# Optimization experiments

Measured on AMD Instinct MI355X. Metric: run time of the kernel, lower is better.

Reference implementation:

```python
import jax, jax.numpy as jnp
import numpy as np
from functools import partial

NUM_GROUP = 512   # S
GROUP_SIZE = 32   # K
BN_EPS = 1e-5
STD_EPS = 1e-5


def fps(xyz, n_samples):
    # xyz: [N,3] -> indices [n_samples] (farthest point sampling, start at idx 0)
    N = xyz.shape[0]
    def body(carry, _):
        dists, last = carry
        d = jnp.sum((xyz - xyz[last]) ** 2, axis=-1)
        dists = jnp.minimum(dists, d)
        nxt = jnp.argmax(dists).astype(jnp.int32)
        return (dists, nxt), last
    init = (jnp.full((N,), jnp.inf, xyz.dtype), jnp.array(0, jnp.int32))
    _, idx = jax.lax.scan(body, init, None, length=n_samples)
    return idx


def knn_idx(xyz, center, k):
    # xyz [N,3], center [S,3] -> k nearest neighbor indices [S,k]
    d2 = (jnp.sum(center ** 2, -1)[:, None] + jnp.sum(xyz ** 2, -1)[None, :]
          - 2.0 * center @ xyz.T)
    _, idx = jax.lax.top_k(-d2, k)
    return idx


def conv1(x, W, b):
    # 1x1 Conv1d: x [M,Cin,L], W [Cout,Cin] -> [M,Cout,L]
    return jnp.einsum('oc,mcl->mol', W, x) + b[None, :, None]


def bn(x, g, b):
    # BatchNorm1d eval mode with running_mean=0, running_var=1
    scale = g / jnp.sqrt(1.0 + BN_EPS)
    return x * scale[None, :, None] + b[None, :, None]


def res_block(x, W1, b1, g1, bb1, W2, b2, g2, bb2):
    # ConvBNReLURes1D, res_expansion=1.0
    h = jax.nn.relu(bn(conv1(x, W1, b1), g1, bb1))
    h = bn(conv1(h, W2, b2), g2, bb2)
    return jax.nn.relu(h + x)


def reference(xyz, alpha, beta, Wt, bt, gt, bbt,
              Wpre1, bpre1, gpre1, bbpre1, Wpre2, bpre2, gpre2, bbpre2,
              Wpos1, bpos1, gpos1, bbpos1, Wpos2, bpos2, gpos2, bbpos2):
    B, N, _ = xyz.shape
    S, K = NUM_GROUP, GROUP_SIZE
    C = Wt.shape[0]

    # ---- LocalGrouper: FPS + KNN + gather + normalize ----
    c_idx = jax.vmap(partial(fps, n_samples=S))(xyz)          # [B,S]
    center = jax.vmap(lambda p, i: p[i])(xyz, c_idx)          # [B,S,3]
    n_idx = jax.vmap(partial(knn_idx, k=K))(xyz, center)      # [B,S,K]
    nbr = jax.vmap(lambda p, i: p[i])(xyz, n_idx)             # [B,S,K,3]

    mean = center[:, :, None, :]
    diff = nbr - mean
    std = jnp.std(diff.reshape(B, -1), axis=-1, ddof=1).reshape(B, 1, 1, 1)
    nbr = alpha * (diff / (std + STD_EPS)) + beta
    grouped = jnp.concatenate(
        [nbr, jnp.broadcast_to(mean, (B, S, K, 3))], axis=-1)  # [B,S,K,6]

    # ---- Extraction ----
    x = grouped.transpose(0, 1, 3, 2).reshape(B * S, 6, K)     # [B*S,6,K]
    h = jax.nn.relu(bn(conv1(x, Wt, bt), gt, bbt))             # [B*S,C,K]
    h = res_block(h, Wpre1, bpre1, gpre1, bbpre1, Wpre2, bpre2, gpre2, bbpre2)
    pooled = jnp.max(h, axis=-1)                               # [B*S,C]
    feat = pooled.reshape(B, S, C).transpose(0, 2, 1)          # [B,C,S]
    feat = res_block(feat, Wpos1, bpos1, gpos1, bbpos1, Wpos2, bpos2, gpos2, bbpos2)
    return feat.transpose(0, 2, 1)                             # [B,S,C]


def setup_inputs() -> dict:
    key = jax.random.key(0)
    ks = jax.random.split(key, 12)
    B, N, C = 8, 8192, 384
    s6 = 1.0 / np.sqrt(6.0)
    sc = 1.0 / np.sqrt(C)
    return {
        'xyz': jax.random.normal(ks[0], (B, N, 3), jnp.float32),
        'alpha': jnp.ones((1, 1, 1, 3), jnp.float32),
        'beta': jnp.zeros((1, 1, 1, 3), jnp.float32),
        'Wt': jax.random.normal(ks[1], (C, 6), jnp.float32) * s6,
        'bt': jax.random.normal(ks[2], (C,), jnp.float32) * 0.02,
        'gt': jnp.ones((C,), jnp.float32), 'bbt': jnp.zeros((C,), jnp.float32),
        'Wpre1': jax.random.normal(ks[3], (C, C), jnp.float32) * sc,
        'bpre1': jax.random.normal(ks[4], (C,), jnp.float32) * 0.02,
        'gpre1': jnp.ones((C,), jnp.float32), 'bbpre1': jnp.zeros((C,), jnp.float32),
        'Wpre2': jax.random.normal(ks[5], (C, C), jnp.float32) * sc,
        'bpre2': jax.random.normal(ks[6], (C,), jnp.float32) * 0.02,
        'gpre2': jnp.ones((C,), jnp.float32), 'bbpre2': jnp.zeros((C,), jnp.float32),
        'Wpos1': jax.random.normal(ks[7], (C, C), jnp.float32) * sc,
        'bpos1': jax.random.normal(ks[8], (C,), jnp.float32) * 0.02,
        'gpos1': jnp.ones((C,), jnp.float32), 'bbpos1': jnp.zeros((C,), jnp.float32),
        'Wpos2': jax.random.normal(ks[9], (C, C), jnp.float32) * sc,
        'bpos2': jax.random.normal(ks[10], (C,), jnp.float32) * 0.02,
        'gpos2': jnp.ones((C,), jnp.float32), 'bbpos2': jnp.zeros((C,), jnp.float32),
    }
```

## Files before the change

kernel.cpp:

```cpp
#include <hip/hip_runtime.h>
#include <hip/hip_bf16.h>
#include <math.h>

typedef __bf16 bf16x8 __attribute__((ext_vector_type(8)));
typedef float f32x4 __attribute__((ext_vector_type(4)));
typedef float f32x2 __attribute__((ext_vector_type(2)));

#define NPTS 8192
#define SGRP 512
#define KNBR 32
#define CCH 384
#define LDSP 392

static __device__ __forceinline__ unsigned short f2b(float f) {
  union { float f; unsigned u; } v; v.f = f;
  return (unsigned short)((v.u + 0x7fffu + ((v.u >> 16) & 1u)) >> 16);
}
static __device__ __forceinline__ float b2f(unsigned short u) {
  union { unsigned u; float f; } v; v.u = ((unsigned)u) << 16;
  return v.f;
}
static __device__ __forceinline__ unsigned pk2(float a, float b) {
  return (unsigned)f2b(a) | ((unsigned)f2b(b) << 16);
}

#define DPPMAX(v, ctrl) \
  fmaxf((v), __int_as_float(__builtin_amdgcn_update_dpp(0, __float_as_int(v), (ctrl), 0xf, 0xf, false)))
#define DPPMIN(v, ctrl) \
  fminf((v), __int_as_float(__builtin_amdgcn_update_dpp(0x7f800000, __float_as_int(v), (ctrl), 0xf, 0xf, false)))

struct FoldArgs {
  const float *W, *b, *g, *bb;
  unsigned short* Wd;
  float* bd;
};
__global__ void fold4_bf16(FoldArgs a0, FoldArgs a1, FoldArgs a2, FoldArgs a3) {
  FoldArgs a = (blockIdx.y == 0) ? a0 : (blockIdx.y == 1) ? a1 : (blockIdx.y == 2) ? a2 : a3;
  int o = blockIdx.x;
  float sc = a.g[o] / sqrtf(1.0f + 1e-5f);
  for (int c = threadIdx.x; c < CCH; c += blockDim.x)
    a.Wd[o * CCH + c] = f2b(a.W[o * CCH + c] * sc);
  if (threadIdx.x == 0) a.bd[o] = a.b[o] * sc + a.bb[o];
}
__global__ void fold_w_f32(const float* __restrict__ W, const float* __restrict__ b,
                           const float* __restrict__ g, const float* __restrict__ bb,
                           float* __restrict__ Wd, float* __restrict__ bd, int Cin) {
  int o = blockIdx.x;
  float sc = g[o] / sqrtf(1.0f + 1e-5f);
  for (int c = threadIdx.x; c < Cin; c += blockDim.x)
    Wd[o * Cin + c] = W[o * Cin + c] * sc;
  if (threadIdx.x == 0) bd[o] = b[o] * sc + bb[o];
}

__global__ __launch_bounds__(1024)
void fps_kernel(const float* __restrict__ xyz, int* __restrict__ cIdx) {
  #pragma clang fp contract(off)
  __shared__ float xs[NPTS], ys[NPTS], zs[NPTS];
  __shared__ float slotV[2][16];
  __shared__ unsigned slotI[2][16];
  const int tid = threadIdx.x, lane = tid & 63, wid = tid >> 6;
  const int b = blockIdx.x;
  const float* xb = xyz + (size_t)b * NPTS * 3;

  f32x2 X2[4], Y2[4], Z2[4], D2[4];
  {
    const float4* s = (const float4*)xb + tid * 6;
    float4 t0 = s[0], t1 = s[1], t2 = s[2], t3 = s[3], t4 = s[4], t5 = s[5];
    X2[0] = (f32x2){t0.x, t0.w}; Y2[0] = (f32x2){t0.y, t1.x}; Z2[0] = (f32x2){t0.z, t1.y};
    X2[1] = (f32x2){t1.z, t2.y}; Y2[1] = (f32x2){t1.w, t2.z}; Z2[1] = (f32x2){t2.x, t2.w};
    X2[2] = (f32x2){t3.x, t3.w}; Y2[2] = (f32x2){t3.y, t4.x}; Z2[2] = (f32x2){t3.z, t4.y};
    X2[3] = (f32x2){t4.z, t5.y}; Y2[3] = (f32x2){t4.w, t5.z}; Z2[3] = (f32x2){t5.x, t5.w};
  }
  #pragma unroll
  for (int j = 0; j < 4; ++j) {
    int p = tid * 8 + j * 2;
    xs[p] = X2[j].x; ys[p] = Y2[j].x; zs[p] = Z2[j].x;
    xs[p + 1] = X2[j].y; ys[p + 1] = Y2[j].y; zs[p + 1] = Z2[j].y;
    D2[j] = (f32x2){__builtin_inff(), __builtin_inff()};
  }
  if (tid == 0) cIdx[b * SGRP] = 0;
  __syncthreads();
  float cx = xs[0], cy = ys[0], cz = zs[0];
  const int tbase = tid * 8;

  for (int step = 1; step < SGRP; ++step) {
    const int par = step & 1;
    const f32x2 cxv = (f32x2){cx, cx}, cyv = (f32x2){cy, cy}, czv = (f32x2){cz, cz};
    float bv = -1.0f; int bi = 0;
    #pragma unroll
    for (int j = 0; j < 4; ++j) {
      f32x2 dx = X2[j] - cxv, dy = Y2[j] - cyv, dz = Z2[j] - czv;
      f32x2 d = (dx * dx + dy * dy) + dz * dz;
      f32x2 nd = __builtin_elementwise_min(D2[j], d);
      D2[j] = nd;
      if (nd.x > bv) { bv = nd.x; bi = tbase + 2 * j; }
      if (nd.y > bv) { bv = nd.y; bi = tbase + 2 * j + 1; }
    }
    float m = bv;
    m = DPPMAX(m, 0x111); m = DPPMAX(m, 0x112); m = DPPMAX(m, 0x114);
    m = DPPMAX(m, 0x118); m = DPPMAX(m, 0x142); m = DPPMAX(m, 0x143);
    float wmax = __uint_as_float(__builtin_amdgcn_readlane(__float_as_uint(m), 63));
    unsigned long long msk = __ballot(bv == wmax);
    int srcLane = (int)__builtin_ctzll(msk);
    unsigned wbi = (unsigned)__builtin_amdgcn_readlane(bi, srcLane);
    if (lane == 0) { slotV[par][wid] = wmax; slotI[par][wid] = wbi; }
    __syncthreads();
    float sv = slotV[par][lane & 15];
    unsigned si = slotI[par][lane & 15];
    float g = sv;
    g = DPPMAX(g, 0x111); g = DPPMAX(g, 0x112); g = DPPMAX(g, 0x114);
    g = DPPMAX(g, 0x118);
    float gm = __uint_as_float(__builtin_amdgcn_readlane(__float_as_uint(g), 15));
    int l0 = (int)__builtin_ctzll(__ballot(sv == gm));
    unsigned gi = (unsigned)__builtin_amdgcn_readlane((int)si, l0);
    if (tid == 0) cIdx[b * SGRP + step] = (int)gi;
    cx = xs[gi]; cy = ys[gi]; cz = zs[gi];
  }
}

__global__ __launch_bounds__(512) void knn_kernel(const float* __restrict__ xyz,
                                                  const int* __restrict__ cIdx,
                                                  float* __restrict__ nbrDiff,
                                                  float* __restrict__ ctrW,
                                                  float* __restrict__ partials) {
  #pragma clang fp contract(off)
  __shared__ unsigned long long keyBuf[4];
  __shared__ int winners[KNBR];
  const int cid = blockIdx.x;
  const int b = cid >> 9;
  const int tid = threadIdx.x;
  const int lane = tid & 63;
  const float* xb = xyz + (size_t)b * NPTS * 3;
  const int cI = cIdx[cid];
  const float cx = xb[cI * 3], cy = xb[cI * 3 + 1], cz = xb[cI * 3 + 2];
  const float cs = (cx * cx + cy * cy) + cz * cz;

  float d2[16];
  float mv = __builtin_inff(); int mi = 0;
  #pragma unroll
  for (int j = 0; j < 16; ++j) {
    int p = tid + (j << 9);
    float x = xb[p * 3], y = xb[p * 3 + 1], z = xb[p * 3 + 2];
    float ps = (x * x + y * y) + z * z;
    float dot = (cx * x + cy * y) + cz * z;
    d2[j] = (cs + ps) - 2.0f * dot;
    if (d2[j] < mv) { mv = d2[j]; mi = p; }
  }
  if (tid < 4) keyBuf[tid] = 0xFFFFFFFFFFFFFFFFull;
  __syncthreads();

  for (int it = 0; it < KNBR; ++it) {
    if (tid == 0) keyBuf[(it + 2) & 3] = 0xFFFFFFFFFFFFFFFFull;
    float m = mv;
    m = DPPMIN(m, 0x111); m = DPPMIN(m, 0x112); m = DPPMIN(m, 0x114);
    m = DPPMIN(m, 0x118); m = DPPMIN(m, 0x142); m = DPPMIN(m, 0x143);
    float wmin = __uint_as_float(__builtin_amdgcn_readlane(__float_as_uint(m), 63));
    unsigned long long msk = __ballot(mv == wmin);
    int src = (int)__builtin_ctzll(msk);
    int wbi = __builtin_amdgcn_readlane(mi, src);
    if (__builtin_popcountll(msk) > 1) {
      unsigned long long rest = msk & (msk - 1);
      while (rest) {
        int l = (int)__builtin_ctzll(rest);
        int cand = __builtin_amdgcn_readlane(mi, l);
        if (cand < wbi) wbi = cand;
        rest &= rest - 1;
      }
    }
    if (lane == 0) {
      unsigned u = __float_as_uint(wmin);
      unsigned mm = u ^ (unsigned)(((int)u >> 31) | 0x80000000);
      unsigned long long key = (((unsigned long long)mm) << 32) | (unsigned long long)(unsigned)wbi;
      atomicMin(&keyBuf[it & 3], key);
    }
    __syncthreads();
    unsigned long long k = keyBuf[it & 3];
    int wi = (int)(k & 0x1FFFu);
    if (tid == 0) winners[it] = wi;
    if (tid == (wi & 511)) {
      #pragma unroll
      for (int j = 0; j < 16; ++j)
        if (wi == tid + (j << 9)) d2[j] = __builtin_inff();
      mv = __builtin_inff(); mi = 0;
      #pragma unroll
      for (int j = 0; j < 16; ++j)
        if (d2[j] < mv) { mv = d2[j]; mi = tid + (j << 9); }
    }
  }
  __syncthreads();

  float sum = 0.f, sq = 0.f;
  if (tid < KNBR) {
    int w = winners[tid];
    float dx = xb[w * 3] - cx, dy = xb[w * 3 + 1] - cy, dz = xb[w * 3 + 2] - cz;
    size_t o = ((size_t)cid * KNBR + tid) * 3;
    nbrDiff[o + 0] = dx; nbrDiff[o + 1] = dy; nbrDiff[o + 2] = dz;
    sum = (dx + dy) + dz;
    sq = (dx * dx + dy * dy) + dz * dz;
  }
  if (tid < 64) {
    #pragma unroll
    for (int s = 1; s < 64; s <<= 1) { sum += __shfl_xor(sum, s); sq += __shfl_xor(sq, s); }
    if (tid == 0) { partials[cid * 2] = sum; partials[cid * 2 + 1] = sq; }
  }
  if (tid < 3) ctrW[(size_t)cid * 3 + tid] = xb[cI * 3 + tid];
}

__global__ __launch_bounds__(256) void std_kernel(const float* __restrict__ partials,
                                                  float* __restrict__ stdv) {
  __shared__ double sd[256], sq[256];
  const int b = blockIdx.x, t = threadIdx.x;
  int i0 = (b * 512 + t) * 2;
  sd[t] = (double)partials[i0] + (double)partials[i0 + 512];
  sq[t] = (double)partials[i0 + 1] + (double)partials[i0 + 513];
  for (int st = 128; st > 0; st >>= 1) {
    __syncthreads();
    if (t < st) { sd[t] += sd[t + st]; sq[t] += sq[t + st]; }
  }
  if (t == 0) {
    double n = (double)(SGRP * KNBR * 3);
    double mean = sd[0] / n;
    double var = (sq[0] - sd[0] * mean) / (n - 1.0);
    stdv[b] = (float)sqrt(var);
  }
}

static __device__ __forceinline__ void gemm_half(const unsigned short* __restrict__ W,
                                                 const unsigned short* ht,
                                                 int oBase, int n0, int r16, int g4,
                                                 f32x4 acc[3][4]) {
  for (int ks = 0; ks < 12; ++ks) {
    const int kOff = ks * 32 + g4 * 8;
    bf16x8 a[3], bb[4];
    #pragma unroll
    for (int i = 0; i < 3; ++i)
      a[i] = *(const bf16x8*)(W + (size_t)(oBase + i * 16 + r16) * CCH + kOff);
    #pragma unroll
    for (int j = 0; j < 4; ++j)
      bb[j] = *(const bf16x8*)(ht + (n0 + j * 16 + r16) * LDSP + kOff);
    #pragma unroll
    for (int i = 0; i < 3; ++i) {
      #pragma unroll
      for (int j = 0; j < 4; ++j)
        acc[i][j] = __builtin_amdgcn_mfma_f32_16x16x32_bf16(a[i], bb[j], acc[i][j], 0, 0, 0);
    }
  }
}

__global__ __launch_bounds__(512) void group_mlp_kernel(
    const float* __restrict__ alpha, const float* __restrict__ beta,
    const float* __restrict__ WtF, const float* __restrict__ btF,
    const unsigned short* __restrict__ W1, const float* __restrict__ b1,
    const unsigned short* __restrict__ W2, const float* __restrict__ b2,
    const float* __restrict__ nbrDiff, const float* __restrict__ ctrW,
    const float* __restrict__ stdv, unsigned short* __restrict__ feat) {
  __shared__ unsigned short ht[128 * LDSP];
  __shared__ float xtw[128 * 8];
  __shared__ float wtl[CCH * 6];
  __shared__ float btl[CCH];

  const int tid = threadIdx.x;
  const int lane = tid & 63, wid = tid >> 6;
  const int r16 = lane & 15, g4 = lane >> 4;
  const int bid = blockIdx.x;
  const int b = bid >> 7;
  const int sBase = (bid & 127) << 2;

  for (int i = tid; i < CCH * 6; i += 512) wtl[i] = WtF[i];
  for (int i = tid; i < CCH; i += 512) btl[i] = btF[i];

  const float inv = 1.0f / (stdv[b] + 1e-5f);
  if (tid < 128) {
    int g = tid >> 5, kk = tid & 31;
    int cid = b * SGRP + sBase + g;
    const float* nb = nbrDiff + ((size_t)cid * KNBR + kk) * 3;
    const float* cc = ctrW + (size_t)cid * 3;
    #pragma unroll
    for (int c = 0; c < 3; ++c) {
      xtw[tid * 8 + c] = alpha[c] * (nb[c] * inv) + beta[c];
      xtw[tid * 8 + 3 + c] = cc[c];
    }
  }
  __syncthreads();

  {
    int l = tid & 127, oi = tid >> 7;
    float xv[6];
    #pragma unroll
    for (int c = 0; c < 6; ++c) xv[c] = xtw[l * 8 + c];
    for (int j = 0; j < 96; ++j) {
      int o = oi * 96 + j;
      float v = btl[o];
      #pragma unroll
      for (int c = 0; c < 6; ++c) v += wtl[o * 6 + c] * xv[c];
      ht[l * LDSP + o] = f2b(fmaxf(v, 0.0f));
    }
  }
  __syncthreads();

  const int oBase = wid * 48;

  for (int half = 0; half < 2; ++half) {
    const int n0 = half * 64;
    f32x4 acc[3][4];
    #pragma unroll
    for (int i = 0; i < 3; ++i) {
      #pragma unroll
      for (int j = 0; j < 4; ++j) acc[i][j] = (f32x4){0.f, 0.f, 0.f, 0.f};
    }
    gemm_half(W1, ht, oBase, n0, r16, g4, acc);
    __syncthreads();
    #pragma unroll
    for (int i = 0; i < 3; ++i) {
      int o4 = oBase + i * 16 + g4 * 4;
      float bs0 = b1[o4], bs1 = b1[o4 + 1], bs2 = b1[o4 + 2], bs3 = b1[o4 + 3];
      #pragma unroll
      for (int j = 0; j < 4; ++j) {
        int row = n0 + j * 16 + r16;
        unsigned u0 = pk2(fmaxf(acc[i][j][0] + bs0, 0.f), fmaxf(acc[i][j][1] + bs1, 0.f));
        unsigned u1 = pk2(fmaxf(acc[i][j][2] + bs2, 0.f), fmaxf(acc[i][j][3] + bs3, 0.f));
        *(uint2*)(ht + row * LDSP + o4) = make_uint2(u0, u1);
      }
    }
    __syncthreads();
  }

  for (int half = 0; half < 2; ++half) {
    const int n0 = half * 64;
    f32x4 acc[3][4];
    #pragma unroll
    for (int i = 0; i < 3; ++i) {
      #pragma unroll
      for (int j = 0; j < 4; ++j) acc[i][j] = (f32x4){0.f, 0.f, 0.f, 0.f};
    }
    gemm_half(W2, ht, oBase, n0, r16, g4, acc);

    float bias2[3][4];
    #pragma unroll
    for (int i = 0; i < 3; ++i) {
      int o4 = oBase + i * 16 + g4 * 4;
      #pragma unroll
      for (int r = 0; r < 4; ++r) bias2[i][r] = b2[o4 + r];
    }
    float mx[3][2][4];
    #pragma unroll
    for (int i = 0; i < 3; ++i) {
      #pragma unroll
      for (int gg = 0; gg < 2; ++gg) {
        #pragma unroll
        for (int r = 0; r < 4; ++r) mx[i][gg][r] = 0.f;
      }
    }
    #pragma unroll
    for (int j = 0; j < 4; ++j) {
      int l = n0 + j * 16 + r16;
      float xv[6];
      #pragma unroll
      for (int c = 0; c < 6; ++c) xv[c] = xtw[l * 8 + c];
      #pragma unroll
      for (int i = 0; i < 3; ++i) {
        int o4 = oBase + i * 16 + g4 * 4;
        #pragma unroll
        for (int r = 0; r < 4; ++r) {
          float h0 = btl[o4 + r];
          #pragma unroll
          for (int c = 0; c < 6; ++c) h0 += wtl[(o4 + r) * 6 + c] * xv[c];
          h0 = fmaxf(h0, 0.f);
          float v = fmaxf(acc[i][j][r] + bias2[i][r] + h0, 0.f);
          mx[i][j >> 1][r] = fmaxf(mx[i][j >> 1][r], v);
        }
      }
    }
    #pragma unroll
    for (int i = 0; i < 3; ++i) {
      #pragma unroll
      for (int gg = 0; gg < 2; ++gg) {
        float m0 = mx[i][gg][0], m1 = mx[i][gg][1], m2 = mx[i][gg][2], m3 = mx[i][gg][3];
        #pragma unroll
        for (int s = 1; s < 16; s <<= 1) {
          m0 = fmaxf(m0, __shfl_xor(m0, s));
          m1 = fmaxf(m1, __shfl_xor(m1, s));
          m2 = fmaxf(m2, __shfl_xor(m2, s));
          m3 = fmaxf(m3, __shfl_xor(m3, s));
        }
        if (r16 == 0) {
          int sIdx = sBase + half * 2 + gg;
          size_t fi = ((size_t)(b * SGRP + sIdx)) * CCH + oBase + i * 16 + g4 * 4;
          *(uint2*)(feat + fi) = make_uint2(pk2(m0, m1), pk2(m2, m3));
        }
      }
    }
  }
}

__global__ __launch_bounds__(256) void pos_kernel(const unsigned short* __restrict__ feat,
                                                  const unsigned short* __restrict__ Wp1,
                                                  const float* __restrict__ bp1,
                                                  const unsigned short* __restrict__ Wp2,
                                                  const float* __restrict__ bp2,
                                                  float* __restrict__ out) {
  __shared__ unsigned short h1[16 * LDSP];
  const int tid = threadIdx.x;
  const int lane = tid & 63, wid = tid >> 6;
  const int r16 = lane & 15, g4 = lane >> 4;
  const int bid = blockIdx.x;
  const int b = bid >> 5;
  const int s0 = (bid & 31) << 4;
  const size_t rowBase = ((size_t)(b * SGRP + s0 + r16)) * CCH;

  f32x4 acc[6];
  #pragma unroll
  for (int i = 0; i < 6; ++i) acc[i] = (f32x4){0.f, 0.f, 0.f, 0.f};
  for (int ks = 0; ks < 12; ++ks) {
    const int kOff = ks * 32 + g4 * 8;
    bf16x8 bfr = *(const bf16x8*)(feat + rowBase + kOff);
    #pragma unroll
    for (int i = 0; i < 6; ++i) {
      bf16x8 a = *(const bf16x8*)(Wp1 + (size_t)(wid * 96 + i * 16 + r16) * CCH + kOff);
      acc[i] = __builtin_amdgcn_mfma_f32_16x16x32_bf16(a, bfr, acc[i], 0, 0, 0);
    }
  }
  #pragma unroll
  for (int i = 0; i < 6; ++i) {
    int o4 = wid * 96 + i * 16 + g4 * 4;
    unsigned u0 = pk2(fmaxf(acc[i][0] + bp1[o4 + 0], 0.f), fmaxf(acc[i][1] + bp1[o4 + 1], 0.f));
    unsigned u1 = pk2(fmaxf(acc[i][2] + bp1[o4 + 2], 0.f), fmaxf(acc[i][3] + bp1[o4 + 3], 0.f));
    *(uint2*)(h1 + r16 * LDSP + o4) = make_uint2(u0, u1);
  }
  __syncthreads();

  f32x4 acc2[6];
  #pragma unroll
  for (int i = 0; i < 6; ++i) acc2[i] = (f32x4){0.f, 0.f, 0.f, 0.f};
  for (int ks = 0; ks < 12; ++ks) {
    const int kOff = ks * 32 + g4 * 8;
    bf16x8 bfr = *(const bf16x8*)(h1 + r16 * LDSP + kOff);
    #pragma unroll
    for (int i = 0; i < 6; ++i) {
      bf16x8 a = *(const bf16x8*)(Wp2 + (size_t)(wid * 96 + i * 16 + r16) * CCH + kOff);
      acc2[i] = __builtin_amdgcn_mfma_f32_16x16x32_bf16(a, bfr, acc2[i], 0, 0, 0);
    }
  }
  #pragma unroll
  for (int i = 0; i < 6; ++i) {
    int o4 = wid * 96 + i * 16 + g4 * 4;
    uint2 rr = *(const uint2*)(feat + rowBase + o4);
    float4 v;
    v.x = fmaxf(acc2[i][0] + bp2[o4 + 0] + b2f((unsigned short)(rr.x & 0xffff)), 0.f);
    v.y = fmaxf(acc2[i][1] + bp2[o4 + 1] + b2f((unsigned short)(rr.x >> 16)), 0.f);
    v.z = fmaxf(acc2[i][2] + bp2[o4 + 2] + b2f((unsigned short)(rr.y & 0xffff)), 0.f);
    v.w = fmaxf(acc2[i][3] + bp2[o4 + 3] + b2f((unsigned short)(rr.y >> 16)), 0.f);
    *(float4*)(out + rowBase + o4) = v;
  }
}

extern "C" void kernel_launch(void* const* d_in, const int* in_sizes, int n_in,
                              void* d_out, int out_size, void* d_ws, size_t ws_size,
                              hipStream_t stream) {
  (void)in_sizes; (void)n_in; (void)out_size; (void)ws_size;
  const float* xyz   = (const float*)d_in[0];
  const float* alpha = (const float*)d_in[1];
  const float* beta  = (const float*)d_in[2];
  const float* Wt    = (const float*)d_in[3];
  const float* bt    = (const float*)d_in[4];
  const float* gt    = (const float*)d_in[5];
  const float* bbt   = (const float*)d_in[6];
  const float* Wpre1 = (const float*)d_in[7];
  const float* bpre1 = (const float*)d_in[8];
  const float* gpre1 = (const float*)d_in[9];
  const float* bbpre1= (const float*)d_in[10];
  const float* Wpre2 = (const float*)d_in[11];
  const float* bpre2 = (const float*)d_in[12];
  const float* gpre2 = (const float*)d_in[13];
  const float* bbpre2= (const float*)d_in[14];
  const float* Wpos1 = (const float*)d_in[15];
  const float* bpos1 = (const float*)d_in[16];
  const float* gpos1 = (const float*)d_in[17];
  const float* bbpos1= (const float*)d_in[18];
  const float* Wpos2 = (const float*)d_in[19];
  const float* bpos2 = (const float*)d_in[20];
  const float* gpos2 = (const float*)d_in[21];
  const float* bbpos2= (const float*)d_in[22];

  char* ws = (char*)d_ws;
  size_t off = 0;
  auto alloc = [&](size_t bytes) -> void* {
    void* p = ws + off;
    off += (bytes + 255) & ~(size_t)255;
    return p;
  };
  float* WtF = (float*)alloc(CCH * 6 * 4);
  float* btF = (float*)alloc(CCH * 4);
  unsigned short* W1 = (unsigned short*)alloc(CCH * CCH * 2);
  float* b1 = (float*)alloc(CCH * 4);
  unsigned short* W2 = (unsigned short*)alloc(CCH * CCH * 2);
  float* b2 = (float*)alloc(CCH * 4);
  unsigned short* Wp1 = (unsigned short*)alloc(CCH * CCH * 2);
  float* bp1 = (float*)alloc(CCH * 4);
  unsigned short* Wp2 = (unsigned short*)alloc(CCH * CCH * 2);
  float* bp2 = (float*)alloc(CCH * 4);
  int* cIdx = (int*)alloc(8 * SGRP * 4);
  float* ctrW = (float*)alloc(8 * SGRP * 3 * 4);
  float* nbrD = (float*)alloc((size_t)8 * SGRP * KNBR * 3 * 4);
  float* partials = (float*)alloc(8 * SGRP * 2 * 4);
  float* stdv = (float*)alloc(8 * 4);
  unsigned short* feat = (unsigned short*)alloc((size_t)8 * SGRP * CCH * 2);

  fold_w_f32<<<CCH, 64, 0, stream>>>(Wt, bt, gt, bbt, WtF, btF, 6);
  FoldArgs fa0{Wpre1, bpre1, gpre1, bbpre1, W1, b1};
  FoldArgs fa1{Wpre2, bpre2, gpre2, bbpre2, W2, b2};
  FoldArgs fa2{Wpos1, bpos1, gpos1, bbpos1, Wp1, bp1};
  FoldArgs fa3{Wpos2, bpos2, gpos2, bbpos2, Wp2, bp2};
  fold4_bf16<<<dim3(CCH, 4), 128, 0, stream>>>(fa0, fa1, fa2, fa3);

  fps_kernel<<<8, 1024, 0, stream>>>(xyz, cIdx);
  knn_kernel<<<8 * SGRP, 512, 0, stream>>>(xyz, cIdx, nbrD, ctrW, partials);
  std_kernel<<<8, 256, 0, stream>>>(partials, stdv);
  group_mlp_kernel<<<1024, 512, 0, stream>>>(alpha, beta, WtF, btF, W1, b1, W2, b2,
                                             nbrD, ctrW, stdv, feat);
  pos_kernel<<<256, 256, 0, stream>>>(feat, Wp1, bp1, Wp2, bp2, (float*)d_out);
}
```

Measured before the change: 959.2 us.

## Replace block-wide per-step KNN selection with per-wave top-K then merge

New measurement: 1.001 ms. 4.4% more time.

```diff
diff --git a/kernel.cpp b/kernel.cpp
--- a/kernel.cpp
+++ b/kernel.cpp
@@ -124,67 +124,95 @@
                                                   float* __restrict__ ctrW,
                                                   float* __restrict__ partials) {
   #pragma clang fp contract(off)
-  __shared__ unsigned long long keyBuf[4];
+  __shared__ float waveV[8 * KNBR];
+  __shared__ int waveI[8 * KNBR];
   __shared__ int winners[KNBR];
   const int cid = blockIdx.x;
   const int b = cid >> 9;
   const int tid = threadIdx.x;
-  const int lane = tid & 63;
+  const int lane = tid & 63, wid = tid >> 6;
   const float* xb = xyz + (size_t)b * NPTS * 3;
   const int cI = cIdx[cid];
   const float cx = xb[cI * 3], cy = xb[cI * 3 + 1], cz = xb[cI * 3 + 2];
   const float cs = (cx * cx + cy * cy) + cz * cz;
 
   float d2[16];
-  float mv = __builtin_inff(); int mi = 0;
-  #pragma unroll
-  for (int j = 0; j < 16; ++j) {
-    int p = tid + (j << 9);
-    float x = xb[p * 3], y = xb[p * 3 + 1], z = xb[p * 3 + 2];
-    float ps = (x * x + y * y) + z * z;
-    float dot = (cx * x + cy * y) + cz * z;
-    d2[j] = (cs + ps) - 2.0f * dot;
-    if (d2[j] < mv) { mv = d2[j]; mi = p; }
-  }
-  if (tid < 4) keyBuf[tid] = 0xFFFFFFFFFFFFFFFFull;
-  __syncthreads();
+  float mv = __builtin_inff(); int mj = 0;
+  {
+    const float4* s = (const float4*)xb + tid * 12;
+    float tmp[48];
+    #pragma unroll
+    for (int q = 0; q < 12; ++q) {
+      float4 t = s[q];
+      tmp[q * 4 + 0] = t.x; tmp[q * 4 + 1] = t.y;
+      tmp[q * 4 + 2] = t.z; tmp[q * 4 + 3] = t.w;
+    }
+    #pragma unroll
+    for (int j = 0; j < 16; ++j) {
+      float x = tmp[j * 3], y = tmp[j * 3 + 1], z = tmp[j * 3 + 2];
+      float ps = (x * x + y * y) + z * z;
+      float dot = (cx * x + cy * y) + cz * z;
+      d2[j] = (cs + ps) - 2.0f * dot;
+      if (d2[j] < mv) { mv = d2[j]; mj = j; }
+    }
+  }
 
   for (int it = 0; it < KNBR; ++it) {
-    if (tid == 0) keyBuf[(it + 2) & 3] = 0xFFFFFFFFFFFFFFFFull;
     float m = mv;
     m = DPPMIN(m, 0x111); m = DPPMIN(m, 0x112); m = DPPMIN(m, 0x114);
     m = DPPMIN(m, 0x118); m = DPPMIN(m, 0x142); m = DPPMIN(m, 0x143);
     float wmin = __uint_as_float(__builtin_amdgcn_readlane(__float_as_uint(m), 63));
     unsigned long long msk = __ballot(mv == wmin);
     int src = (int)__builtin_ctzll(msk);
-    int wbi = __builtin_amdgcn_readlane(mi, src);
-    if (__builtin_popcountll(msk) > 1) {
-      unsigned long long rest = msk & (msk - 1);
-      while (rest) {
-        int l = (int)__builtin_ctzll(rest);
-        int cand = __builtin_amdgcn_readlane(mi, l);
-        if (cand < wbi) wbi = cand;
-        rest &= rest - 1;
+    int mjs = __builtin_amdgcn_readlane(mj, src);
+    if (lane == 0) {
+      waveV[wid * KNBR + it] = wmin;
+      waveI[wid * KNBR + it] = (wid << 10) + (src << 4) + mjs;
+    }
+    if (lane == src) {
+      #pragma unroll
+      for (int j = 0; j < 16; ++j)
+        if (j == mjs) d2[j] = __builtin_inff();
+      mv = __builtin_inff(); mj = 0;
+      #pragma unroll
+      for (int j = 0; j < 16; ++j)
+        if (d2[j] < mv) { mv = d2[j]; mj = j; }
+    }
+  }
+  __syncthreads();
+
+  if (wid == 0) {
+    float v[4]; int ix[4];
+    #pragma unroll
+    for (int q = 0; q < 4; ++q) {
+      v[q] = waveV[lane * 4 + q];
+      ix[q] = waveI[lane * 4 + q];
+    }
+    for (int it = 0; it < KNBR; ++it) {
+      float bv = __builtin_inff(); int bi = 0x7fffffff;
+      #pragma unroll
+      for (int q = 0; q < 4; ++q)
+        if (v[q] < bv || (v[q] == bv && ix[q] < bi)) { bv = v[q]; bi = ix[q]; }
+      float m = bv;
+      m = DPPMIN(m, 0x111); m = DPPMIN(m, 0x112); m = DPPMIN(m, 0x114);
+      m = DPPMIN(m, 0x118); m = DPPMIN(m, 0x142); m = DPPMIN(m, 0x143);
+      float wmin = __uint_as_float(__builtin_amdgcn_readlane(__float_as_uint(m), 63));
+      unsigned long long msk = __ballot(bv == wmin);
+      int src = (int)__builtin_ctzll(msk);
+      int chosen = __builtin_amdgcn_readlane(bi, src);
+      if (__builtin_popcountll(msk) > 1) {
+        unsigned long long rest = msk & (msk - 1);
+        while (rest) {
+          int l = (int)__builtin_ctzll(rest);
+          int cand = __builtin_amdgcn_readlane(bi, l);
+          if (cand < chosen) chosen = cand;
+          rest &= rest - 1;
+        }
       }
-    }
-    if (lane == 0) {
-      unsigned u = __float_as_uint(wmin);
-      unsigned mm = u ^ (unsigned)(((int)u >> 31) | 0x80000000);
-      unsigned long long key = (((unsigned long long)mm) << 32) | (unsigned long long)(unsigned)wbi;
-      atomicMin(&keyBuf[it & 3], key);
-    }
-    __syncthreads();
-    unsigned long long k = keyBuf[it & 3];
-    int wi = (int)(k & 0x1FFFu);
-    if (tid == 0) winners[it] = wi;
-    if (tid == (wi & 511)) {
-      #pragma unroll
-      for (int j = 0; j < 16; ++j)
-        if (wi == tid + (j << 9)) d2[j] = __builtin_inff();
-      mv = __builtin_inff(); mi = 0;
-      #pragma unroll
-      for (int j = 0; j < 16; ++j)
-        if (d2[j] < mv) { mv = d2[j]; mi = tid + (j << 9); }
+      if (lane == 0) winners[it] = chosen;
+      #pragma unroll
+      for (int q = 0; q < 4; ++q)
+        if (ix[q] == chosen) v[q] = __builtin_inff();
     }
   }
   __syncthreads();
@@ -288,12 +316,17 @@
     float xv[6];
     #pragma unroll
     for (int c = 0; c < 6; ++c) xv[c] = xtw[l * 8 + c];
-    for (int j = 0; j < 96; ++j) {
-      int o = oi * 96 + j;
-      float v = btl[o];
-      #pragma unroll
-      for (int c = 0; c < 6; ++c) v += wtl[o * 6 + c] * xv[c];
-      ht[l * LDSP + o] = f2b(fmaxf(v, 0.0f));
+    for (int j4 = 0; j4 < 24; ++j4) {
+      int o = oi * 96 + j4 * 4;
+      float vv[4];
+      #pragma unroll
+      for (int r = 0; r < 4; ++r) {
+        float v = btl[o + r];
+        #pragma unroll
+        for (int c = 0; c < 6; ++c) v += wtl[(o + r) * 6 + c] * xv[c];
+        vv[r] = fmaxf(v, 0.0f);
+      }
+      *(uint2*)(ht + l * LDSP + o) = make_uint2(pk2(vv[0], vv[1]), pk2(vv[2], vv[3]));
     }
   }
   __syncthreads();
```
